# Kernel tuning notes

Measured on AMD Instinct MI355X. Metric: run time of the kernel, lower is better.

The kernel has to match this reference:

```python
import jax, jax.numpy as jnp
import numpy as np

B, S, D, H, L = 32, 1024, 512, 8, 4
DH = D // H
FF = D            # dim_feedforward == hidden_dim in the original ctor call
LOC_D, TD_D = 16, 8
TD_EMB = 3        # time_dist_embed_dim
POI = 21          # poi vocab
POI_EMB = 3
ADDR_IN = 1 + POI_EMB
FC = 32           # fc_hidden_dim
NEG = -1e9


def setup_inputs() -> dict:
    key = jax.random.key(0)
    ks = jax.random.split(key, 20)
    g = lambda i, shape, s=0.02: jax.random.normal(ks[i], shape, jnp.float32) * s
    return {
        "addr": jax.random.normal(ks[0], (B, 1), jnp.float32),
        "loc_dense_seq": jax.random.normal(ks[1], (B, S, LOC_D), jnp.float32),
        "time_dist_seq": jax.random.normal(ks[2], (B, S, TD_D), jnp.float32),
        "Wtd": g(3, (TD_D, TD_EMB)), "btd": jnp.zeros((TD_EMB,), jnp.float32),
        "Wemb": g(4, (LOC_D + TD_EMB, D)), "bemb": jnp.zeros((D,), jnp.float32),
        "Wqkv": g(5, (L, D, 3 * D)), "bqkv": jnp.zeros((L, 3 * D), jnp.float32),
        "Wo": g(6, (L, D, D)), "bo": jnp.zeros((L, D), jnp.float32),
        "ln1_g": jnp.ones((L, D), jnp.float32), "ln1_b": jnp.zeros((L, D), jnp.float32),
        "W1": g(7, (L, D, FF)), "b1": jnp.zeros((L, FF), jnp.float32),
        "W2": g(8, (L, FF, D)), "b2": jnp.zeros((L, D), jnp.float32),
        "ln2_g": jnp.ones((L, D), jnp.float32), "ln2_b": jnp.zeros((L, D), jnp.float32),
        "poi_emb": g(9, (POI, POI_EMB), 1.0),
        "Wa": g(10, (ADDR_IN, FC)), "ba": jnp.zeros((FC,), jnp.float32),
        "Wout": g(11, (D, FC)),
        "Wcomb": g(12, (FC, 1)),
        "addr_type": jax.random.randint(ks[13], (B, 1), 0, POI),
        "data_length": jax.random.randint(ks[14], (B,), 1, S + 1),
    }


def _ln(x, g, b, eps=1e-5):
    m = x.mean(-1, keepdims=True)
    v = ((x - m) ** 2).mean(-1, keepdims=True)
    return (x - m) / jnp.sqrt(v + eps) * g + b


def reference(addr, loc_dense_seq, time_dist_seq, Wtd, btd, Wemb, bemb, Wqkv,
              bqkv, Wo, bo, ln1_g, ln1_b, W1, b1, W2, b2, ln2_g, ln2_b,
              poi_emb, Wa, ba, Wout, Wcomb, addr_type, data_length):
    valid = jnp.arange(S)[None, :] < data_length[:, None]            # [B,S]
    td = time_dist_seq @ Wtd + btd                                   # [B,S,3]
    x = jnp.concatenate([loc_dense_seq, td], axis=-1) @ Wemb + bemb  # [B,S,D]
    scale = 1.0 / jnp.sqrt(jnp.float32(DH))
    for l in range(L):  # post-norm TransformerEncoderLayer (relu, eval/no-dropout)
        qkv = x @ Wqkv[l] + bqkv[l]
        q, k, v = jnp.split(qkv, 3, axis=-1)
        q = q.reshape(B, S, H, DH)
        k = k.reshape(B, S, H, DH)
        v = v.reshape(B, S, H, DH)
        scores = jnp.einsum('bqhd,bkhd->bhqk', q, k) * scale
        scores = jnp.where(valid[:, None, None, :], scores, NEG)     # mask padded keys
        attn = jax.nn.softmax(scores, axis=-1)
        ctx = jnp.einsum('bhqk,bkhd->bqhd', attn, v).reshape(B, S, D)
        x = _ln(x + ctx @ Wo[l] + bo[l], ln1_g[l], ln1_b[l])
        ff = jax.nn.relu(x @ W1[l] + b1[l]) @ W2[l] + b2[l]
        x = _ln(x + ff, ln2_g[l], ln2_b[l])
    # per-sample addr branch (vectorized over the original python loop)
    addr_inp = jnp.concatenate([addr, poi_emb[addr_type[:, 0]]], axis=-1)  # [B,4]
    a = addr_inp @ Wa + ba                                                 # [B,FC]
    o = (jnp.tanh(x @ Wout + a[:, None, :]) @ Wcomb)[..., 0]              # [B,S]
    logits = jnp.where(valid, o, NEG)
    logp = jax.nn.log_softmax(logits, axis=1)  # log_softmax over valid positions only
    return jnp.where(valid, logp, 0.0)
```

## Files before the change

### kernel.cpp

```cpp
#include <hip/hip_runtime.h>
#include <stdint.h>


typedef unsigned short u16;
typedef __attribute__((ext_vector_type(8))) short short8;
typedef __attribute__((ext_vector_type(4))) float f32x4;

constexpr int Bn = 32, Sn = 1024, Dn = 512, Ln = 4;
constexpr int BS = Bn * Sn;

__device__ __forceinline__ float b2f(u16 u) {
    union { uint32_t i; float f; } v; v.i = ((uint32_t)u) << 16; return v.f;
}
__device__ __forceinline__ u16 f2b(float f) {
    union { float f; uint32_t i; } v; v.f = f;
    uint32_t r = v.i + 0x7fffu + ((v.i >> 16) & 1u);
    return (u16)(r >> 16);
}
__device__ __forceinline__ float getf(const void* p, size_t i, int F) {
    return F ? ((const float*)p)[i] : b2f(((const u16*)p)[i]);
}
__device__ __forceinline__ void cp16(void* lds, const void* g) {
    __builtin_amdgcn_global_load_lds(
        (__attribute__((address_space(1))) void*)(uintptr_t)g,
        (__attribute__((address_space(3))) void*)(uint32_t)(uintptr_t)lds,
        16, 0, 0);
}

__global__ __launch_bounds__(256)
void detect_kernel(const void* loc, int* flag)
{
    __shared__ int cnt;
    if (threadIdx.x == 0) cnt = 0;
    __syncthreads();
    const u16* p = (const u16*)loc;
    int c = 0;
    for (int i = threadIdx.x; i < 2048; i += 256) {
        const float v = b2f(p[i]);
        if (!(fabsf(v) <= 100.0f)) c++;
    }
    atomicAdd(&cnt, c);
    __syncthreads();
    if (threadIdx.x == 0) *flag = (cnt >= 64) ? 1 : 0;
}

__global__ __launch_bounds__(256)
void gemm_bt(const u16* __restrict__ A, const u16* __restrict__ Bt,
             const void* __restrict__ bias, int boff, u16* __restrict__ C,
             int N, int K, int relu, const int* __restrict__ flagp,
             const int* __restrict__ dlen)
{
    __shared__ __align__(16) u16 As[128 * 32];
    __shared__ __align__(16) u16 Bs[128 * 32];
    const int bn0 = blockIdx.x * 128, bm0 = blockIdx.y * 128;
    if ((bm0 & 1023) >= dlen[bm0 >> 10]) return;
    const int F = *flagp;
    const int tid = threadIdx.x;
    const int lane = tid & 63, w = tid >> 6;
    const int wm = w >> 1, wn = w & 1;
    const int quad = lane >> 4, l16 = lane & 15;

    const f32x4 vzero = {0.f, 0.f, 0.f, 0.f};
    f32x4 acc[4][4];
#pragma unroll
    for (int i = 0; i < 4; i++)
#pragma unroll
        for (int j = 0; j < 4; j++) acc[i][j] = vzero;

    const int i0 = tid, i1 = tid + 256;
    const u16* a0 = A + (size_t)(bm0 + (i0 >> 2)) * K + (i0 & 3) * 8;
    const u16* a1 = A + (size_t)(bm0 + (i1 >> 2)) * K + (i1 & 3) * 8;
    const u16* b0 = Bt + (size_t)(bn0 + (i0 >> 2)) * K + (i0 & 3) * 8;
    const u16* b1 = Bt + (size_t)(bn0 + (i1 >> 2)) * K + (i1 & 3) * 8;

    for (int k0 = 0; k0 < K; k0 += 32) {
        cp16(As + i0 * 8, a0 + k0);
        cp16(As + i1 * 8, a1 + k0);
        cp16(Bs + i0 * 8, b0 + k0);
        cp16(Bs + i1 * 8, b1 + k0);
        __syncthreads();
        short8 af[4], bfr[4];
#pragma unroll
        for (int t = 0; t < 4; t++)
            af[t] = *(const short8*)&As[(wm * 64 + t * 16 + l16) * 32 + quad * 8];
#pragma unroll
        for (int t = 0; t < 4; t++)
            bfr[t] = *(const short8*)&Bs[(wn * 64 + t * 16 + l16) * 32 + quad * 8];
#pragma unroll
        for (int tm = 0; tm < 4; tm++)
#pragma unroll
            for (int tn = 0; tn < 4; tn++)
                acc[tm][tn] = __builtin_amdgcn_mfma_f32_16x16x32_bf16(
                    af[tm], bfr[tn], acc[tm][tn], 0, 0, 0);
        __syncthreads();
    }
#pragma unroll
    for (int tm = 0; tm < 4; tm++)
#pragma unroll
        for (int tn = 0; tn < 4; tn++) {
            const int col = bn0 + wn * 64 + tn * 16 + l16;
            const float bv = getf(bias, (size_t)boff + col, F);
#pragma unroll
            for (int r = 0; r < 4; r++) {
                const int row = bm0 + wm * 64 + tm * 16 + quad * 4 + r;
                float v = acc[tm][tn][r] + bv;
                if (relu) v = fmaxf(v, 0.0f);
                C[(size_t)row * N + col] = f2b(v);
            }
        }
}

__global__ __launch_bounds__(256)
void attn_kernel(const u16* __restrict__ qkv, const int* __restrict__ dlen,
                 u16* __restrict__ ctx)
{
    const int id = blockIdx.x;
    const int qt = id >> 8;
    const int bh = id & 255;
    const int h = bh & 7, b = bh >> 3;
    const int len = dlen[b];
    if (qt * 128 >= len) return;
    const int tid = threadIdx.x, lane = tid & 63, w = tid >> 6;
    const int quad = lane >> 4, l16 = lane & 15;
    __shared__ __align__(16) u16 Vt[64 * 72];
    __shared__ __align__(16) u16 Pl[4][16 * 64];
    const size_t rs = 3 * Dn;
    const u16* base = qkv + (size_t)b * Sn * rs;
    const int q0 = qt * 128 + w * 32;

    short8 qf[2][2];
#pragma unroll
    for (int sub = 0; sub < 2; sub++)
#pragma unroll
        for (int s = 0; s < 2; s++)
            qf[sub][s] = *(const short8*)(base + (size_t)(q0 + sub * 16 + l16) * rs
                                          + h * 64 + quad * 8 + 32 * s);

    const f32x4 vzero = {0.f, 0.f, 0.f, 0.f};
    f32x4 O[2][4];
    float ls[2][4];
#pragma unroll
    for (int sub = 0; sub < 2; sub++)
#pragma unroll
        for (int t = 0; t < 4; t++) { O[sub][t] = vzero; ls[sub][t] = 0.f; }

    const int nkt = (len + 63) >> 6;
    for (int kt = 0; kt < nkt; kt++) {
        const int k0 = kt * 64;
        {
            const int key = tid >> 2, f0 = (tid & 3) * 16;
            const u16* vp = base + (size_t)(k0 + key) * rs + 2 * Dn + h * 64 + f0;
            short8 v0 = *(const short8*)vp;
            short8 v1 = *(const short8*)(vp + 8);
#pragma unroll
            for (int j = 0; j < 8; j++) {
                Vt[(f0 + j) * 72 + key]     = (u16)v0[j];
                Vt[(f0 + 8 + j) * 72 + key] = (u16)v1[j];
            }
        }
        __syncthreads();

        short8 kf[4][2];
#pragma unroll
        for (int tn = 0; tn < 4; tn++) {
            const u16* kp = base + (size_t)(k0 + tn * 16 + l16) * rs + Dn
                            + h * 64 + quad * 8;
            kf[tn][0] = *(const short8*)kp;
            kf[tn][1] = *(const short8*)(kp + 32);
        }

#pragma unroll
        for (int sub = 0; sub < 2; sub++) {
            f32x4 sacc[4];
#pragma unroll
            for (int tn = 0; tn < 4; tn++) {
                f32x4 z = vzero;
                z = __builtin_amdgcn_mfma_f32_16x16x32_bf16(qf[sub][0], kf[tn][0], z, 0, 0, 0);
                sacc[tn] = __builtin_amdgcn_mfma_f32_16x16x32_bf16(qf[sub][1], kf[tn][1], z, 0, 0, 0);
            }
#pragma unroll
            for (int tn = 0; tn < 4; tn++) {
                const bool ok = (k0 + tn * 16 + l16) < len;
#pragma unroll
                for (int r = 0; r < 4; r++) {
                    const float p = ok ? __expf(sacc[tn][r] * 0.125f) : 0.0f;
                    ls[sub][r] += p;
                    Pl[w][(quad * 4 + r) * 64 + tn * 16 + l16] = f2b(p);
                }
            }
#pragma unroll
            for (int s = 0; s < 2; s++) {
                short8 pf = *(const short8*)&Pl[w][l16 * 64 + quad * 8 + 32 * s];
#pragma unroll
                for (int t = 0; t < 4; t++) {
                    short8 vf = *(const short8*)&Vt[(t * 16 + l16) * 72 + quad * 8 + 32 * s];
                    O[sub][t] = __builtin_amdgcn_mfma_f32_16x16x32_bf16(pf, vf, O[sub][t], 0, 0, 0);
                }
            }
        }
        __syncthreads();
    }
#pragma unroll
    for (int sub = 0; sub < 2; sub++)
#pragma unroll
        for (int r = 0; r < 4; r++) {
#pragma unroll
            for (int o = 1; o < 16; o <<= 1)
                ls[sub][r] += __shfl_xor(ls[sub][r], o, 64);
        }
#pragma unroll
    for (int sub = 0; sub < 2; sub++)
#pragma unroll
        for (int t = 0; t < 4; t++)
#pragma unroll
            for (int r = 0; r < 4; r++) {
                const int q = q0 + sub * 16 + quad * 4 + r;
                ctx[(size_t)(b * Sn + q) * Dn + h * 64 + t * 16 + l16] =
                    f2b(O[sub][t][r] / ls[sub][r]);
            }
}

__global__ __launch_bounds__(256)
void ln_res(u16* __restrict__ x, const u16* __restrict__ t,
            const void* __restrict__ g, const void* __restrict__ bta, int off,
            const int* __restrict__ flagp, const int* __restrict__ dlen)
{
    const int w = threadIdx.x >> 6, lane = threadIdx.x & 63;
    const size_t row = (size_t)blockIdx.x * 4 + w;
    if ((int)(row & 1023) >= dlen[row >> 10]) return;
    const int F = *flagp;
    u16* xp = x + row * Dn;
    const u16* tp = t + row * Dn;
    const int c0 = lane * 8;
    short8 xv = *(const short8*)(xp + c0);
    short8 tv = *(const short8*)(tp + c0);
    float v[8]; float s = 0.f;
#pragma unroll
    for (int i = 0; i < 8; i++) {
        v[i] = b2f((u16)xv[i]) + b2f((u16)tv[i]);
        s += v[i];
    }
#pragma unroll
    for (int o = 1; o < 64; o <<= 1) s += __shfl_xor(s, o, 64);
    const float mean = s * (1.0f / 512.0f);
    float q = 0.f;
#pragma unroll
    for (int i = 0; i < 8; i++) { const float d = v[i] - mean; q += d * d; }
#pragma unroll
    for (int o = 1; o < 64; o <<= 1) q += __shfl_xor(q, o, 64);
    const float inv = rsqrtf(q * (1.0f / 512.0f) + 1e-5f);
    short8 ov;
#pragma unroll
    for (int i = 0; i < 8; i++)
        ov[i] = (short)f2b((v[i] - mean) * inv * getf(g, off + c0 + i, F)
                           + getf(bta, off + c0 + i, F));
    *(short8*)(xp + c0) = ov;
}

__global__ __launch_bounds__(256)
void embed_kernel(const void* __restrict__ loc, const void* __restrict__ tds,
                  const void* __restrict__ Wtd, const void* __restrict__ btd,
                  const void* __restrict__ Wemb, const void* __restrict__ bemb,
                  u16* __restrict__ x, const int* __restrict__ flagp,
                  const int* __restrict__ dlen)
{
    const int token = blockIdx.x;
    if ((token & 1023) >= dlen[token >> 10]) return;
    const int F = *flagp;
    const int tid = threadIdx.x;
    __shared__ float inv[19];
    if (tid < 16) {
        inv[tid] = getf(loc, (size_t)token * 16 + tid, F);
    } else if (tid < 19) {
        const int e = tid - 16;
        float a = getf(btd, e, F);
        for (int j = 0; j < 8; j++)
            a += getf(tds, (size_t)token * 8 + j, F) * getf(Wtd, j * 3 + e, F);
        inv[tid] = a;
    }
    __syncthreads();
    for (int d = tid; d < Dn; d += 256) {
        float a = getf(bemb, d, F);
#pragma unroll
        for (int i = 0; i < 19; i++) a += inv[i] * getf(Wemb, (size_t)i * Dn + d, F);
        x[(size_t)token * Dn + d] = f2b(a);
    }
}

__global__ __launch_bounds__(256)
void transpose_w(const void* __restrict__ src, u16* __restrict__ dst,
                 int K, int N, const int* __restrict__ flagp)
{
    const int F = *flagp;
    __shared__ u16 tile[32][33];
    const size_t ls = (size_t)K * N;
    const size_t sb = (size_t)blockIdx.z * ls;
    u16* d = dst + blockIdx.z * ls;
    const int tx = threadIdx.x & 31, ty = threadIdx.x >> 5;
    const int n0 = blockIdx.x * 32, k0 = blockIdx.y * 32;
#pragma unroll
    for (int i = 0; i < 32; i += 8)
        tile[ty + i][tx] = f2b(getf(src, sb + (size_t)(k0 + ty + i) * N + n0 + tx, F));
    __syncthreads();
#pragma unroll
    for (int i = 0; i < 32; i += 8)
        d[(size_t)(n0 + ty + i) * K + k0 + tx] = tile[tx][ty + i];
}

__global__ __launch_bounds__(256)
void final_proj(const u16* __restrict__ x, const void* __restrict__ Wout,
                const void* __restrict__ Wcomb, const void* __restrict__ addr,
                const void* __restrict__ poi, const int* __restrict__ atype,
                const void* __restrict__ Wa, const void* __restrict__ ba,
                float* __restrict__ logits, const int* __restrict__ flagp,
                const int* __restrict__ dlen)
{
    const int F = *flagp;
    __shared__ float xs[8][512];
    const int tid = threadIdx.x;
    const int t0 = blockIdx.x * 8;
    for (int i = tid; i < 8 * 512; i += 256) {
        const int tk = i >> 9, d = i & 511;
        xs[tk][d] = b2f(x[(size_t)(t0 + tk) * Dn + d]);
    }
    __syncthreads();
    const int half = tid >> 5, j = tid & 31;
    const int token = t0 + half;
    const int b = token >> 10;
    if ((token & 1023) >= dlen[b]) return;
    const int ty = atype[b];
    float a = getf(ba, j, F) + getf(addr, b, F) * getf(Wa, j, F);
#pragma unroll
    for (int e = 0; e < 3; e++)
        a += getf(poi, ty * 3 + e, F) * getf(Wa, (1 + e) * 32 + j, F);
    float s = a;
    for (int k = 0; k < 512; k++) s += xs[half][k] * getf(Wout, (size_t)k * 32 + j, F);
    float o = tanhf(s) * getf(Wcomb, j, F);
#pragma unroll
    for (int off = 1; off < 32; off <<= 1) o += __shfl_xor(o, off, 64);
    if (j == 0) logits[token] = o;
}

__global__ __launch_bounds__(256)
void lsm_kernel(const float* __restrict__ logits, const int* __restrict__ dlen,
                float* __restrict__ out)
{
    const int b = blockIdx.x, tid = threadIdx.x;
    const int len = dlen[b];
    const float* lp = logits + (size_t)b * Sn;
    __shared__ float wA[4], wB[4];
    float mx = -3e38f;
    for (int s = tid; s < Sn; s += 256) if (s < len) mx = fmaxf(mx, lp[s]);
#pragma unroll
    for (int o = 1; o < 64; o <<= 1) mx = fmaxf(mx, __shfl_xor(mx, o, 64));
    if ((tid & 63) == 0) wA[tid >> 6] = mx;
    __syncthreads();
    mx = fmaxf(fmaxf(wA[0], wA[1]), fmaxf(wA[2], wA[3]));
    float sm = 0.f;
    for (int s = tid; s < Sn; s += 256) if (s < len) sm += __expf(lp[s] - mx);
#pragma unroll
    for (int o = 1; o < 64; o <<= 1) sm += __shfl_xor(sm, o, 64);
    if ((tid & 63) == 0) wB[tid >> 6] = sm;
    __syncthreads();
    const float lse = mx + __logf(wB[0] + wB[1] + wB[2] + wB[3]);
    for (int s = tid; s < Sn; s += 256)
        out[(size_t)b * Sn + s] = (s < len) ? (lp[s] - lse) : 0.0f;
}

extern "C" void kernel_launch(void* const* d_in, const int* in_sizes, int n_in,
                              void* d_out, int out_size, void* d_ws, size_t ws_size,
                              hipStream_t stream) {
    const void* addr  = d_in[0];
    const void* loc   = d_in[1];
    const void* tds   = d_in[2];
    const void* Wtd   = d_in[3];
    const void* btd   = d_in[4];
    const void* Wemb  = d_in[5];
    const void* bemb  = d_in[6];
    const void* Wqkv  = d_in[7];
    const void* bqkv  = d_in[8];
    const void* Wo    = d_in[9];
    const void* bo    = d_in[10];
    const void* ln1g  = d_in[11];
    const void* ln1b  = d_in[12];
    const void* W1    = d_in[13];
    const void* b1    = d_in[14];
    const void* W2    = d_in[15];
    const void* b2    = d_in[16];
    const void* ln2g  = d_in[17];
    const void* ln2b  = d_in[18];
    const void* poi   = d_in[19];
    const void* Wa    = d_in[20];
    const void* ba    = d_in[21];
    const void* Wout  = d_in[22];
    const void* Wcomb = d_in[23];
    const int* atype  = (const int*)d_in[24];
    const int* dlen   = (const int*)d_in[25];

    char* base = (char*)d_ws;
    u16*   xb    = (u16*)(base);
    u16*   qkvb  = (u16*)(base + 33554432ull);
    u16*   ctxb  = (u16*)(base + 134217728ull);
    u16*   tb    = (u16*)(base + 167772160ull);
    u16*   wqkvT = (u16*)(base + 201326592ull);
    u16*   woT   = (u16*)(base + 207618048ull);
    u16*   w1T   = (u16*)(base + 209715200ull);
    u16*   w2T   = (u16*)(base + 211812352ull);
    float* logit = (float*)(base + 213909504ull);
    int*   flag  = (int*)  (base + 214040576ull);
    if (ws_size < 214040592ull) return;

    detect_kernel<<<1, 256, 0, stream>>>(loc, flag);

    transpose_w<<<dim3(48, 16, 4), 256, 0, stream>>>(Wqkv, wqkvT, 512, 1536, flag);
    transpose_w<<<dim3(16, 16, 4), 256, 0, stream>>>(Wo,   woT,   512, 512, flag);
    transpose_w<<<dim3(16, 16, 4), 256, 0, stream>>>(W1,   w1T,   512, 512, flag);
    transpose_w<<<dim3(16, 16, 4), 256, 0, stream>>>(W2,   w2T,   512, 512, flag);

    embed_kernel<<<BS, 256, 0, stream>>>(loc, tds, Wtd, btd, Wemb, bemb, xb, flag, dlen);

    for (int l = 0; l < Ln; l++) {
        gemm_bt<<<dim3(12, 256), 256, 0, stream>>>(
            xb, wqkvT + (size_t)l * 1536 * 512, bqkv, l * 1536, qkvb, 1536, 512, 0, flag, dlen);
        attn_kernel<<<2048, 256, 0, stream>>>(qkvb, dlen, ctxb);
        gemm_bt<<<dim3(4, 256), 256, 0, stream>>>(
            ctxb, woT + (size_t)l * 512 * 512, bo, l * 512, tb, 512, 512, 0, flag, dlen);
        ln_res<<<BS / 4, 256, 0, stream>>>(xb, tb, ln1g, ln1b, l * 512, flag, dlen);
        gemm_bt<<<dim3(4, 256), 256, 0, stream>>>(
            xb, w1T + (size_t)l * 512 * 512, b1, l * 512, ctxb, 512, 512, 1, flag, dlen);
        gemm_bt<<<dim3(4, 256), 256, 0, stream>>>(
            ctxb, w2T + (size_t)l * 512 * 512, b2, l * 512, tb, 512, 512, 0, flag, dlen);
        ln_res<<<BS / 4, 256, 0, stream>>>(xb, tb, ln2g, ln2b, l * 512, flag, dlen);
    }

    final_proj<<<BS / 8, 256, 0, stream>>>(xb, Wout, Wcomb, addr, poi, atype,
                                           Wa, ba, logit, flag, dlen);
    lsm_kernel<<<Bn, 256, 0, stream>>>(logit, dlen, (float*)d_out);
}
```

Measured before the change: 1.793 ms.

## Pre-transpose V into global buffer and remove block barriers from attention

Adds a vtrans kernel that writes V transposed per (batch, head) into a scratch buffer. The attention kernel then reads V fragments straight from global memory instead of rebuilding a shared-memory transpose on every key tile, which lets it drop both __syncthreads in favour of per-wave barriers. QK^T is computed with swapped operands so each lane writes probabilities as packed, XOR-swizzled words into LDS and only two row sums need reducing. final_proj now stages Wout transposed in LDS as bf16 before its dot-product loop. The cost is one extra kernel launch plus a global round trip for V in each layer, and final_proj loses precision when the weights arrive as fp32.

```diff
diff --git a/kernel.cpp b/kernel.cpp
--- a/kernel.cpp
+++ b/kernel.cpp
@@ -111,8 +111,33 @@
 }
 
 __global__ __launch_bounds__(256)
-void attn_kernel(const u16* __restrict__ qkv, const int* __restrict__ dlen,
-                 u16* __restrict__ ctx)
+void vtrans(const u16* __restrict__ qkv, const int* __restrict__ dlen,
+            u16* __restrict__ vt)
+{
+    const int kt = blockIdx.x, bh = blockIdx.y;
+    const int b = bh >> 3, h = bh & 7;
+    if (kt * 64 >= dlen[b]) return;
+    __shared__ __align__(16) u16 T[64 * 72];
+    const int tid = threadIdx.x;
+    const u16* src = qkv + (size_t)b * Sn * 1536 + 2 * Dn + h * 64;
+    const int key2 = (tid & 31) * 2, f0 = (tid >> 5) * 8;
+    const u16* p0 = src + (size_t)(kt * 64 + key2) * 1536 + f0;
+    short8 v0 = *(const short8*)p0;
+    short8 v1 = *(const short8*)(p0 + 1536);
+#pragma unroll
+    for (int j = 0; j < 8; j++) {
+        const uint32_t pk = (uint32_t)(u16)v0[j] | ((uint32_t)(u16)v1[j] << 16);
+        *(uint32_t*)&T[(f0 + j) * 72 + key2] = pk;
+    }
+    __syncthreads();
+    const int feat = tid >> 2, kc = tid & 3;
+    short8 r = *(const short8*)&T[feat * 72 + kc * 16];
+    *(short8*)(vt + ((size_t)(bh * 64 + feat)) * Sn + kt * 64 + kc * 16) = r;
+}
+
+__global__ __launch_bounds__(256)
+void attn_kernel(const u16* __restrict__ qkv, const u16* __restrict__ vt,
+                 const int* __restrict__ dlen, u16* __restrict__ ctx)
 {
     const int id = blockIdx.x;
     const int qt = id >> 8;
@@ -122,10 +147,12 @@
     if (qt * 128 >= len) return;
     const int tid = threadIdx.x, lane = tid & 63, w = tid >> 6;
     const int quad = lane >> 4, l16 = lane & 15;
-    __shared__ __align__(16) u16 Vt[64 * 72];
-    __shared__ __align__(16) u16 Pl[4][16 * 64];
+    __shared__ __align__(16) u16 Pl[4][32 * 72];
+    u16* Plw = Pl[w];
+    const int sw = l16 & 3;
     const size_t rs = 3 * Dn;
     const u16* base = qkv + (size_t)b * Sn * rs;
+    const u16* vbase = vt + (size_t)(bh * 64) * Sn;
     const int q0 = qt * 128 + w * 32;
 
     short8 qf[2][2];
@@ -138,28 +165,15 @@
 
     const f32x4 vzero = {0.f, 0.f, 0.f, 0.f};
     f32x4 O[2][4];
-    float ls[2][4];
+    float ls[2] = {0.f, 0.f};
 #pragma unroll
     for (int sub = 0; sub < 2; sub++)
 #pragma unroll
-        for (int t = 0; t < 4; t++) { O[sub][t] = vzero; ls[sub][t] = 0.f; }
+        for (int t = 0; t < 4; t++) O[sub][t] = vzero;
 
     const int nkt = (len + 63) >> 6;
     for (int kt = 0; kt < nkt; kt++) {
         const int k0 = kt * 64;
-        {
-            const int key = tid >> 2, f0 = (tid & 3) * 16;
-            const u16* vp = base + (size_t)(k0 + key) * rs + 2 * Dn + h * 64 + f0;
-            short8 v0 = *(const short8*)vp;
-            short8 v1 = *(const short8*)(vp + 8);
-#pragma unroll
-            for (int j = 0; j < 8; j++) {
-                Vt[(f0 + j) * 72 + key]     = (u16)v0[j];
-                Vt[(f0 + 8 + j) * 72 + key] = (u16)v1[j];
-            }
-        }
-        __syncthreads();
-
         short8 kf[4][2];
 #pragma unroll
         for (int tn = 0; tn < 4; tn++) {
@@ -168,56 +182,64 @@
             kf[tn][0] = *(const short8*)kp;
             kf[tn][1] = *(const short8*)(kp + 32);
         }
-
+        __builtin_amdgcn_wave_barrier();
 #pragma unroll
         for (int sub = 0; sub < 2; sub++) {
             f32x4 sacc[4];
 #pragma unroll
             for (int tn = 0; tn < 4; tn++) {
                 f32x4 z = vzero;
-                z = __builtin_amdgcn_mfma_f32_16x16x32_bf16(qf[sub][0], kf[tn][0], z, 0, 0, 0);
-                sacc[tn] = __builtin_amdgcn_mfma_f32_16x16x32_bf16(qf[sub][1], kf[tn][1], z, 0, 0, 0);
+                z = __builtin_amdgcn_mfma_f32_16x16x32_bf16(kf[tn][0], qf[sub][0], z, 0, 0, 0);
+                sacc[tn] = __builtin_amdgcn_mfma_f32_16x16x32_bf16(kf[tn][1], qf[sub][1], sacc[tn] = z, 0, 0, 0);
             }
+            const int prow = (sub * 16 + l16) * 72;
 #pragma unroll
             for (int tn = 0; tn < 4; tn++) {
-                const bool ok = (k0 + tn * 16 + l16) < len;
+                const int kb = k0 + tn * 16 + quad * 4;
+                float p[4];
 #pragma unroll
                 for (int r = 0; r < 4; r++) {
-                    const float p = ok ? __expf(sacc[tn][r] * 0.125f) : 0.0f;
-                    ls[sub][r] += p;
-                    Pl[w][(quad * 4 + r) * 64 + tn * 16 + l16] = f2b(p);
+                    p[r] = (kb + r < len) ? __expf(sacc[tn][r] * 0.125f) : 0.0f;
+                    ls[sub] += p[r];
                 }
-            }
-#pragma unroll
-            for (int s = 0; s < 2; s++) {
-                short8 pf = *(const short8*)&Pl[w][l16 * 64 + quad * 8 + 32 * s];
-#pragma unroll
-                for (int t = 0; t < 4; t++) {
-                    short8 vf = *(const short8*)&Vt[(t * 16 + l16) * 72 + quad * 8 + 32 * s];
-                    O[sub][t] = __builtin_amdgcn_mfma_f32_16x16x32_bf16(pf, vf, O[sub][t], 0, 0, 0);
-                }
+                uint2 pk;
+                pk.x = (uint32_t)f2b(p[0]) | ((uint32_t)f2b(p[1]) << 16);
+                pk.y = (uint32_t)f2b(p[2]) | ((uint32_t)f2b(p[3]) << 16);
+                *(uint2*)&Plw[prow + ((tn ^ sw) << 4) + quad * 4] = pk;
             }
         }
-        __syncthreads();
+        __builtin_amdgcn_wave_barrier();
+#pragma unroll
+        for (int s = 0; s < 2; s++) {
+            const int tnr = ((quad >> 1) + 2 * s) ^ sw;
+            short8 pf0 = *(const short8*)&Plw[(l16) * 72 + (tnr << 4) + (quad & 1) * 8];
+            short8 pf1 = *(const short8*)&Plw[(16 + l16) * 72 + (tnr << 4) + (quad & 1) * 8];
+#pragma unroll
+            for (int t = 0; t < 4; t++) {
+                short8 vf = *(const short8*)(vbase + (size_t)(t * 16 + l16) * Sn
+                                             + k0 + quad * 8 + 32 * s);
+                O[0][t] = __builtin_amdgcn_mfma_f32_16x16x32_bf16(pf0, vf, O[0][t], 0, 0, 0);
+                O[1][t] = __builtin_amdgcn_mfma_f32_16x16x32_bf16(pf1, vf, O[1][t], 0, 0, 0);
+            }
+        }
+    }
+#pragma unroll
+    for (int sub = 0; sub < 2; sub++) {
+        ls[sub] += __shfl_xor(ls[sub], 16, 64);
+        ls[sub] += __shfl_xor(ls[sub], 32, 64);
     }
 #pragma unroll
     for (int sub = 0; sub < 2; sub++)
 #pragma unroll
         for (int r = 0; r < 4; r++) {
-#pragma unroll
-            for (int o = 1; o < 16; o <<= 1)
-                ls[sub][r] += __shfl_xor(ls[sub][r], o, 64);
+            const float lv = __shfl(ls[sub], quad * 4 + r, 64);
+            const float inv = 1.0f / lv;
+            const int q = q0 + sub * 16 + quad * 4 + r;
+#pragma unroll
+            for (int t = 0; t < 4; t++)
+                ctx[(size_t)(b * Sn + q) * Dn + h * 64 + t * 16 + l16] =
+                    f2b(O[sub][t][r] * inv);
         }
-#pragma unroll
-    for (int sub = 0; sub < 2; sub++)
-#pragma unroll
-        for (int t = 0; t < 4; t++)
-#pragma unroll
-            for (int r = 0; r < 4; r++) {
-                const int q = q0 + sub * 16 + quad * 4 + r;
-                ctx[(size_t)(b * Sn + q) * Dn + h * 64 + t * 16 + l16] =
-                    f2b(O[sub][t][r] / ls[sub][r]);
-            }
 }
 
 __global__ __launch_bounds__(256)
@@ -317,11 +339,17 @@
 {
     const int F = *flagp;
     __shared__ float xs[8][512];
+    __shared__ u16 wlds[32 * 514];
     const int tid = threadIdx.x;
     const int t0 = blockIdx.x * 8;
     for (int i = tid; i < 8 * 512; i += 256) {
         const int tk = i >> 9, d = i & 511;
         xs[tk][d] = b2f(x[(size_t)(t0 + tk) * Dn + d]);
+    }
+    for (int i = tid; i < 16384; i += 256) {
+        const int k = i >> 5, j = i & 31;
+        wlds[j * 514 + k] = F ? f2b(((const float*)Wout)[(size_t)k * 32 + j])
+                              : ((const u16*)Wout)[(size_t)k * 32 + j];
     }
     __syncthreads();
     const int half = tid >> 5, j = tid & 31;
@@ -334,7 +362,10 @@
     for (int e = 0; e < 3; e++)
         a += getf(poi, ty * 3 + e, F) * getf(Wa, (1 + e) * 32 + j, F);
     float s = a;
-    for (int k = 0; k < 512; k++) s += xs[half][k] * getf(Wout, (size_t)k * 32 + j, F);
+    const u16* wj = wlds + j * 514;
+    const float* xr = xs[half];
+#pragma unroll 8
+    for (int k = 0; k < 512; k++) s += xr[k] * b2f(wj[k]);
     float o = tanhf(s) * getf(Wcomb, j, F);
 #pragma unroll
     for (int off = 1; off < 32; off <<= 1) o += __shfl_xor(o, off, 64);
@@ -422,7 +453,8 @@
     for (int l = 0; l < Ln; l++) {
         gemm_bt<<<dim3(12, 256), 256, 0, stream>>>(
             xb, wqkvT + (size_t)l * 1536 * 512, bqkv, l * 1536, qkvb, 1536, 512, 0, flag, dlen);
-        attn_kernel<<<2048, 256, 0, stream>>>(qkvb, dlen, ctxb);
+        vtrans<<<dim3(16, 256), 256, 0, stream>>>(qkvb, dlen, tb);
+        attn_kernel<<<2048, 256, 0, stream>>>(qkvb, tb, dlen, ctxb);
         gemm_bt<<<dim3(4, 256), 256, 0, stream>>>(
             ctxb, woT + (size_t)l * 512 * 512, bo, l * 512, tb, 512, 512, 0, flag, dlen);
         ln_res<<<BS / 4, 256, 0, stream>>>(xb, tb, ln1g, ln1b, l * 512, flag, dlen);
```

Result: slower. 1.978 ms (+10.3%).
